# Performance work log

Hardware: AMD Instinct MI355X
Metric: run time of the kernel (lower is better)

Reference implementation:

```python
import jax, jax.numpy as jnp
import numpy as np

R = 2          # pool ratio -> context window = R * P
P = 8          # patch_size
STRIDE = 8     # window_stride
NH = 8         # n_heads
EPS = 1e-6


def _partition_nonoverlap(x, ws):
    # (N,C,H,W) -> (N*nH*nW, C, ws, ws), matches F.unfold path with padding 0
    n, c, h, w = x.shape
    x = x.reshape(n, c, h // ws, ws, w // ws, ws)
    x = jnp.transpose(x, (0, 2, 4, 1, 3, 5))
    return x.reshape(-1, c, ws, ws)


def _partition_overlap(x, ws, stride):
    # (N,C,H,W) -> (N*nH*nW, C, ws, ws) with padding (ws-stride)//2, matching F.unfold
    n, c, h, w = x.shape
    pad = (ws - stride) // 2
    xp = jnp.pad(x, ((0, 0), (0, 0), (pad, pad), (pad, pad)))
    ih = (jnp.arange(h // stride) * stride)[:, None] + jnp.arange(ws)[None, :]
    iw = (jnp.arange(w // stride) * stride)[:, None] + jnp.arange(ws)[None, :]
    xw = xp[:, :, ih, :]          # (n, c, nH, ws, Wp)
    xw = xw[:, :, :, :, iw]       # (n, c, nH, ws, nW, ws)
    xw = jnp.transpose(xw, (0, 2, 4, 1, 3, 5))  # (n, nH, nW, c, ws, ws)
    return xw.reshape(-1, c, ws, ws)


def setup_inputs() -> dict:
    key = jax.random.key(0)
    ks = jax.random.split(key, 4)
    C = 512
    x = jax.random.normal(ks[0], (1, C, 128, 128), jnp.float32)
    ln_w = jnp.ones((C,), jnp.float32)
    ln_b = jnp.zeros((C,), jnp.float32)
    mix_w = jax.random.normal(ks[1], (NH, P * P, P * P), jnp.float32) * 0.02
    mix_b = jnp.zeros((NH, P * P), jnp.float32)
    in_w = jax.random.normal(ks[2], (3 * C, C), jnp.float32) * 0.02
    in_b = jnp.zeros((3 * C,), jnp.float32)
    out_w = jax.random.normal(ks[3], (C, C), jnp.float32) * 0.02
    out_b = jnp.zeros((C,), jnp.float32)
    return dict(x=x, ln_w=ln_w, ln_b=ln_b, mix_w=mix_w, mix_b=mix_b,
                in_w=in_w, in_b=in_b, out_w=out_w, out_b=out_b)


def reference(x, ln_w, ln_b, mix_w, mix_b, in_w, in_b, out_w, out_b):
    n, c, h, w = x.shape
    ws = R * P
    L = P * P  # 64 positions per window

    # query windows: non-overlapping 8x8 patches -> (B, L, C)
    q = _partition_nonoverlap(x, P)
    q = q.reshape(-1, c, L).transpose(0, 2, 1)

    # context windows: 16x16 overlapping, avg-pooled r x r -> 8x8 -> (B, L, C)
    ctx = _partition_overlap(x, ws, STRIDE)
    ctx = ctx.reshape(-1, c, P, R, P, R).mean(axis=(3, 5))  # AvgPool2d(r, r)
    ctx = ctx.reshape(-1, c, L).transpose(0, 2, 1)

    # LayerNorm over channel dim (eps 1e-6, biased variance)
    mu = ctx.mean(-1, keepdims=True)
    var = ctx.var(-1, keepdims=True)
    ctx = (ctx - mu) / jnp.sqrt(var + EPS) * ln_w + ln_b

    # PositionMixing: per-head Linear(64,64) over the L axis + residual
    B = ctx.shape[0]
    t = ctx.transpose(0, 2, 1).reshape(B, NH, c // NH, L)  # (B, H, hd, L)
    mixed = jnp.einsum('bhcl,hml->bhcm', t, mix_w) + mix_b[None, :, None, :]
    ctx = (t + mixed).reshape(B, c, L).transpose(0, 2, 1)  # (B, L, C)

    # nn.MultiheadAttention with batch_first=False (torch default):
    # first dim B (windows) is the SEQUENCE, second dim L=64 is the BATCH.
    hd = c // NH
    Wq, Wk, Wv = in_w[:c], in_w[c:2 * c], in_w[2 * c:]
    bq, bk, bv = in_b[:c], in_b[c:2 * c], in_b[2 * c:]
    Q = (jnp.einsum('slc,ec->sle', q, Wq) + bq).reshape(B, L, NH, hd)
    K = (jnp.einsum('slc,ec->sle', ctx, Wk) + bk).reshape(B, L, NH, hd)
    V = (jnp.einsum('slc,ec->sle', ctx, Wv) + bv).reshape(B, L, NH, hd)
    scale = 1.0 / jnp.sqrt(jnp.asarray(hd, x.dtype))
    scores = jnp.einsum('slhd,tlhd->lhst', Q, K) * scale  # (L, H, B, B)
    attn = jax.nn.softmax(scores, axis=-1)
    o = jnp.einsum('lhst,tlhd->slhd', attn, V).reshape(B, L, c)
    o = jnp.einsum('slc,ec->sle', o, out_w) + out_b

    # nlc_to_nchw + window_reverse -> (N, C, H, W)
    o = o.transpose(0, 2, 1).reshape(B, c, P, P)
    o = o.reshape(n, h // P, w // P, c, P, P)
    o = jnp.transpose(o, (0, 3, 1, 4, 2, 5)).reshape(n, c, h, w)
    return o
```

## Files before the change

### kernel.cpp

```cpp
#include <hip/hip_runtime.h>


typedef __bf16 bf16;
typedef __bf16 bf16x2 __attribute__((ext_vector_type(2)));
typedef __bf16 bf16x4 __attribute__((ext_vector_type(4)));
typedef __bf16 bf16x8 __attribute__((ext_vector_type(8)));
typedef float f32x4 __attribute__((ext_vector_type(4)));

#define MFMA(a, b, c) __builtin_amdgcn_mfma_f32_16x16x32_bf16(a, b, c, 0, 0, 0)

__device__ __forceinline__ void gll16(const void* g, void* l) {
  __builtin_amdgcn_global_load_lds((const __attribute__((address_space(1))) void*)g,
                                   (__attribute__((address_space(3))) void*)l, 16, 0, 0);
}

__global__ void k_wconv(const float* __restrict__ in_w, const float* __restrict__ out_w,
                        bf16* __restrict__ wib, bf16* __restrict__ wob) {
  int i = blockIdx.x * blockDim.x + threadIdx.x;
  const int n1 = (1536 * 512) / 4;
  float4 v;
  bf16* dst;
  if (i < n1) { v = ((const float4*)in_w)[i];      dst = wib + (size_t)i * 4; }
  else        { v = ((const float4*)out_w)[i - n1]; dst = wob + (size_t)(i - n1) * 4; }
  dst[0] = (bf16)v.x; dst[1] = (bf16)v.y; dst[2] = (bf16)v.z; dst[3] = (bf16)v.w;
}

__global__ __launch_bounds__(256) void k_pq(const float* __restrict__ x,
                                            float* __restrict__ xp2t,
                                            bf16* __restrict__ qb) {
  __shared__ float xs[2][64][133];
  const int y2 = blockIdx.x, c0 = blockIdx.y * 64, t = threadIdx.x;
  #pragma unroll
  for (int it = 0; it < 16; ++it) {
    int flat = it * 256 + t;
    int ci = flat >> 6, rest = flat & 63;
    int yb = rest >> 5, xq = rest & 31;
    float4 v = *(const float4*)(x + (size_t)(c0 + ci) * 16384 +
                                (size_t)(2 * y2 + yb) * 128 + xq * 4);
    float* d = &xs[yb][ci][xq * 4];
    d[0] = v.x; d[1] = v.y; d[2] = v.z; d[3] = v.w;
  }
  __syncthreads();
  #pragma unroll
  for (int it = 0; it < 16; ++it) {
    int flat = it * 256 + t;
    int x2 = flat >> 6, ci = flat & 63;
    float s = xs[0][ci][2 * x2] + xs[0][ci][2 * x2 + 1] +
              xs[1][ci][2 * x2] + xs[1][ci][2 * x2 + 1];
    xp2t[(size_t)(y2 * 64 + x2) * 512 + c0 + ci] = 0.25f * s;
  }
  #pragma unroll
  for (int yb = 0; yb < 2; ++yb) {
    const int Y = 2 * y2 + yb;
    const int hy = Y >> 3, py = Y & 7;
    #pragma unroll
    for (int it = 0; it < 32; ++it) {
      int flat = it * 256 + t;
      int X = flat >> 6, ci = flat & 63;
      int l = py * 8 + (X & 7), s = hy * 16 + (X >> 3);
      qb[((size_t)l * 256 + s) * 512 + c0 + ci] = (bf16)xs[yb][ci][X];
    }
  }
}

__global__ __launch_bounds__(512) void k_ln(const float* __restrict__ xp2t,
                                            const float* __restrict__ lnw,
                                            const float* __restrict__ lnb,
                                            bf16* __restrict__ T) {
  __shared__ bf16 Tt[512][24];
  const int s = blockIdx.x, qt = blockIdx.y;
  const int wy = s >> 4, wx = s & 15;
  const int t = threadIdx.x, wv = t >> 6, ln = t & 63;

  float wl[8], bl[8];
  #pragma unroll
  for (int k = 0; k < 8; ++k) { wl[k] = lnw[k * 64 + ln]; bl[k] = lnb[k * 64 + ln]; }

  float v[2][8], mu_[2], rs_[2];
  #pragma unroll
  for (int p = 0; p < 2; ++p) {
    const int l = qt * 16 + wv * 2 + p;
    const int py = l >> 3, px = l & 7;
    const int y2 = wy * 4 - 2 + py, x2 = wx * 4 - 2 + px;
    const bool inb = (y2 >= 0) && (y2 < 64) && (x2 >= 0) && (x2 < 64);
    const float* src = xp2t + (size_t)(y2 * 64 + x2) * 512;
    float sum = 0.f, ssq = 0.f;
    #pragma unroll
    for (int k = 0; k < 8; ++k) {
      float xv = 0.f;
      if (inb) xv = src[k * 64 + ln];
      v[p][k] = xv; sum += xv; ssq += xv * xv;
    }
    #pragma unroll
    for (int off = 1; off < 64; off <<= 1) {
      sum += __shfl_xor(sum, off);
      ssq += __shfl_xor(ssq, off);
    }
    float mu = sum * (1.f / 512.f);
    mu_[p] = mu;
    rs_[p] = rsqrtf(ssq * (1.f / 512.f) - mu * mu + 1e-6f);
  }
  #pragma unroll
  for (int k = 0; k < 8; ++k) {
    const int c = k * 64 + ln;
    bf16x2 u;
    u.x = (bf16)((v[0][k] - mu_[0]) * rs_[0] * wl[k] + bl[k]);
    u.y = (bf16)((v[1][k] - mu_[1]) * rs_[1] * wl[k] + bl[k]);
    *(bf16x2*)(&Tt[c][wv * 2]) = u;
  }
  __syncthreads();
  #pragma unroll
  for (int it = 0; it < 2; ++it) {
    int flat = it * 512 + t;
    int c = flat >> 1, ch = flat & 1;
    bf16x8 u = *(const bf16x8*)(&Tt[c][ch * 8]);
    *(bf16x8*)(T + ((size_t)s * 512 + c) * 64 + qt * 16 + ch * 8) = u;
  }
}

__global__ __launch_bounds__(256) void k_mix(const bf16* __restrict__ T,
                                             const float* __restrict__ mix_w,
                                             const float* __restrict__ mix_b,
                                             bf16* __restrict__ ctx) {
  const int t = threadIdx.x, wv = t >> 6, ln = t & 63;
  const int s = blockIdx.x, hg = blockIdx.y;
  const int h = hg * 4 + wv;
  const int q = ln >> 4, r = ln & 15;

  bf16x8 a[4][2];
  #pragma unroll
  for (int m = 0; m < 4; ++m) {
    #pragma unroll
    for (int ks = 0; ks < 2; ++ks) {
      const int rm = m * 16 + r;
      const float* wsrc = mix_w + ((size_t)h * 64 + rm) * 64 + ks * 32 + q * 8;
      bf16x8 pk;
      #pragma unroll
      for (int e = 0; e < 8; ++e) {
        int l = ks * 32 + q * 8 + e;
        float w = wsrc[e] + (rm == l ? 1.f : 0.f);
        pk[e] = (bf16)w;
      }
      a[m][ks] = pk;
    }
  }
  const bf16* Tb = T + ((size_t)s * 512 + h * 64) * 64;
  bf16x8 b[4][2];
  #pragma unroll
  for (int n = 0; n < 4; ++n) {
    #pragma unroll
    for (int ks = 0; ks < 2; ++ks)
      b[n][ks] = *(const bf16x8*)(Tb + (size_t)(n * 16 + r) * 64 + ks * 32 + q * 8);
  }
  f32x4 acc[4][4] = {};
  #pragma unroll
  for (int ks = 0; ks < 2; ++ks) {
    #pragma unroll
    for (int m = 0; m < 4; ++m) {
      #pragma unroll
      for (int n = 0; n < 4; ++n) acc[m][n] = MFMA(a[m][ks], b[n][ks], acc[m][n]);
    }
  }
  #pragma unroll
  for (int m = 0; m < 4; ++m) {
    #pragma unroll
    for (int j = 0; j < 4; ++j) {
      const int rm = m * 16 + q * 4 + j;
      const float bias = mix_b[h * 64 + rm];
      #pragma unroll
      for (int n = 0; n < 4; ++n)
        ctx[((size_t)rm * 256 + s) * 512 + h * 64 + n * 16 + r] =
            (bf16)(acc[m][n][j] + bias);
    }
  }
}

__global__ __launch_bounds__(256, 4) void k_gemmQKV(const bf16* __restrict__ qb,
                                                    const bf16* __restrict__ ctxb,
                                                    const bf16* __restrict__ wib,
                                                    const float* __restrict__ in_b,
                                                    bf16* __restrict__ Qa,
                                                    bf16* __restrict__ Ka,
                                                    bf16* __restrict__ Vt) {
  __shared__ bf16 As[8192];
  __shared__ bf16 Bs[8192];
  const int t = threadIdx.x, wv = t >> 6, ln = t & 63;
  const int bm = blockIdx.x, bny = blockIdx.y;
  const bool isQ = (bny < 4);
  const int bn = isQ ? bny : bny - 4;
  const bf16* A = isQ ? qb : ctxb;
  const bf16* B = isQ ? wib : wib + 512 * 512;
  const float* bias = isQ ? in_b : in_b + 512;
  const int wm = wv >> 1, wn = wv & 1;
  const int q = ln >> 4, r = ln & 15;
  f32x4 acc[4][4] = {};

  const int srow = wv * 8 + (ln >> 3);
  const int swzc = (ln & 7) ^ (ln >> 3);
  const char* ga = (const char*)A + ((size_t)(bm * 128 + srow) * 512) * 2 + swzc * 16;
  const char* gb = (const char*)B + ((size_t)(bn * 128 + srow) * 512) * 2 + swzc * 16;

  for (int k0 = 0; k0 < 512; k0 += 64) {
    #pragma unroll
    for (int i = 0; i < 4; ++i) {
      gll16(ga + (size_t)i * 32 * 1024 + k0 * 2, As + i * 2048 + wv * 512);
      gll16(gb + (size_t)i * 32 * 1024 + k0 * 2, Bs + i * 2048 + wv * 512);
    }
    __syncthreads();
    #pragma unroll
    for (int ks = 0; ks < 2; ++ks) {
      bf16x8 af[4], bfr[4];
      #pragma unroll
      for (int m = 0; m < 4; ++m)
        af[m] = *(const bf16x8*)(As + (wm * 64 + m * 16 + r) * 64 +
                                 (((ks * 4 + q) ^ (r & 7)) * 8));
      #pragma unroll
      for (int n = 0; n < 4; ++n)
        bfr[n] = *(const bf16x8*)(Bs + (wn * 64 + n * 16 + r) * 64 +
                                  (((ks * 4 + q) ^ (r & 7)) * 8));
      #pragma unroll
      for (int m = 0; m < 4; ++m) {
        #pragma unroll
        for (int n = 0; n < 4; ++n) acc[m][n] = MFMA(af[m], bfr[n], acc[m][n]);
      }
    }
    __syncthreads();
  }

  const int r0 = bm * 128 + wm * 64 + q * 4;
  const int c0 = bn * 128 + wn * 64 + r;
  #pragma unroll
  for (int m = 0; m < 4; ++m) {
    const int rg0 = r0 + m * 16;
    const int li = rg0 >> 8;
    #pragma unroll
    for (int n = 0; n < 4; ++n) {
      const int cg = c0 + n * 16;
      const float bv = bias[cg];
      if (isQ) {
        #pragma unroll
        for (int j = 0; j < 4; ++j) {
          int sp = (rg0 + j) & 255;
          Qa[(((size_t)li * 8 + (cg >> 6)) * 256 + sp) * 64 + (cg & 63)] =
              (bf16)(acc[m][n][j] + bv);
        }
      } else if (cg < 512) {
        #pragma unroll
        for (int j = 0; j < 4; ++j) {
          int sp = (rg0 + j) & 255;
          Ka[(((size_t)li * 8 + (cg >> 6)) * 256 + sp) * 64 + (cg & 63)] =
              (bf16)(acc[m][n][j] + bv);
        }
      } else {
        const int e = cg - 512, hh = e >> 6, d = e & 63;
        const int sp = rg0 & 255;
        bf16x4 pk;
        #pragma unroll
        for (int j = 0; j < 4; ++j) pk[j] = (bf16)(acc[m][n][j] + bv);
        *(bf16x4*)(&Vt[(((size_t)li * 8 + hh) * 64 + d) * 256 + sp]) = pk;
      }
    }
  }
}

__global__ __launch_bounds__(256, 4) void k_gemmO(const bf16* __restrict__ A,
                                                  const bf16* __restrict__ B,
                                                  const float* __restrict__ bias,
                                                  bf16* __restrict__ O0) {
  __shared__ bf16 As[8192];
  __shared__ bf16 Bs[8192];
  const int t = threadIdx.x, wv = t >> 6, ln = t & 63;
  const int bm = blockIdx.x, bn = blockIdx.y;
  const int wm = wv >> 1, wn = wv & 1;
  const int q = ln >> 4, r = ln & 15;
  f32x4 acc[4][4] = {};

  const int srow = wv * 8 + (ln >> 3);
  const int swzc = (ln & 7) ^ (ln >> 3);
  const char* ga = (const char*)A + ((size_t)(bm * 128 + srow) * 512) * 2 + swzc * 16;
  const char* gb = (const char*)B + ((size_t)(bn * 128 + srow) * 512) * 2 + swzc * 16;

  for (int k0 = 0; k0 < 512; k0 += 64) {
    #pragma unroll
    for (int i = 0; i < 4; ++i) {
      gll16(ga + (size_t)i * 32 * 1024 + k0 * 2, As + i * 2048 + wv * 512);
      gll16(gb + (size_t)i * 32 * 1024 + k0 * 2, Bs + i * 2048 + wv * 512);
    }
    __syncthreads();
    #pragma unroll
    for (int ks = 0; ks < 2; ++ks) {
      bf16x8 af[4], bfr[4];
      #pragma unroll
      for (int m = 0; m < 4; ++m)
        af[m] = *(const bf16x8*)(As + (wm * 64 + m * 16 + r) * 64 +
                                 (((ks * 4 + q) ^ (r & 7)) * 8));
      #pragma unroll
      for (int n = 0; n < 4; ++n)
        bfr[n] = *(const bf16x8*)(Bs + (wn * 64 + n * 16 + r) * 64 +
                                  (((ks * 4 + q) ^ (r & 7)) * 8));
      #pragma unroll
      for (int m = 0; m < 4; ++m) {
        #pragma unroll
        for (int n = 0; n < 4; ++n) acc[m][n] = MFMA(af[m], bfr[n], acc[m][n]);
      }
    }
    __syncthreads();
  }

  const int r0 = bm * 128 + wm * 64 + q * 4;
  const int c0 = bn * 128 + wn * 64 + r;
  #pragma unroll
  for (int m = 0; m < 4; ++m) {
    const int rg0 = r0 + m * 16;
    #pragma unroll
    for (int n = 0; n < 4; ++n) {
      const int cg = c0 + n * 16;
      const float bv = bias[cg];
      #pragma unroll
      for (int j = 0; j < 4; ++j)
        O0[(size_t)(rg0 + j) * 512 + cg] = (bf16)(acc[m][n][j] + bv);
    }
  }
}

__global__ __launch_bounds__(256, 4) void k_attn(const bf16* __restrict__ Qa,
                                                 const bf16* __restrict__ Ka,
                                                 const bf16* __restrict__ Vt,
                                                 bf16* __restrict__ Oa) {
  __shared__ bf16 Ks[128][68];
  __shared__ bf16 Ps[64][132];
  __shared__ float sfl[64];
  __shared__ float rrs[64];

  const int t = threadIdx.x, wv = t >> 6, ln = t & 63;
  const int q = ln >> 4, r = ln & 15;
  const int bid = blockIdx.x;
  const int st = (bid >> 3) & 3;
  const int lh = (bid & 7) | ((bid >> 5) << 3);
  const int s0 = st * 64;
  const size_t base = (size_t)lh * (256 * 64);
  const bf16* Qlh = Qa + base;
  const bf16* Klh = Ka + base;
  const bf16* Vlh = Vt + base;

  const float SC = 0.125f * 1.4426950408889634f;

  bf16x8 aq[2];
  #pragma unroll
  for (int ks = 0; ks < 2; ++ks)
    aq[ks] = *(const bf16x8*)(Qlh + (size_t)(s0 + wv * 16 + r) * 64 + ks * 32 + q * 8);

  const int krow = t >> 1, khf = (t & 1) * 32;
  {
    bf16x8 kst0[4];
    #pragma unroll
    for (int i = 0; i < 4; ++i)
      kst0[i] = *(const bf16x8*)(Klh + (size_t)krow * 64 + khf + i * 8);
    #pragma unroll
    for (int i = 0; i < 4; ++i) *(bf16x8*)(&Ks[krow][khf + i * 8]) = kst0[i];
  }
  __syncthreads();

  f32x4 ao[4] = {};
  float m4[4], l4[4];
  f32x4 acc[8];

  #pragma unroll
  for (int n = 0; n < 8; ++n) acc[n] = (f32x4){0.f, 0.f, 0.f, 0.f};
  __builtin_amdgcn_s_setprio(1);
  #pragma unroll
  for (int n = 0; n < 8; ++n) {
    bf16x8 b0 = *(const bf16x8*)(&Ks[n * 16 + r][q * 8]);
    bf16x8 b1 = *(const bf16x8*)(&Ks[n * 16 + r][32 + q * 8]);
    acc[n] = MFMA(aq[0], b0, acc[n]);
    acc[n] = MFMA(aq[1], b1, acc[n]);
  }
  __builtin_amdgcn_s_setprio(0);

  bf16x8 bv[4];
  #pragma unroll
  for (int ks = 0; ks < 4; ++ks)
    bv[ks] = *(const bf16x8*)(Vlh + (size_t)(wv * 16 + r) * 256 + ks * 32 + q * 8);
  bf16x8 kst[4];
  #pragma unroll
  for (int i = 0; i < 4; ++i)
    kst[i] = *(const bf16x8*)(Klh + (size_t)(128 + krow) * 64 + khf + i * 8);

  #pragma unroll
  for (int j = 0; j < 4; ++j) {
    float mx = acc[0][j];
    #pragma unroll
    for (int n = 1; n < 8; ++n) mx = fmaxf(mx, acc[n][j]);
    #pragma unroll
    for (int off = 1; off < 16; off <<= 1) mx = fmaxf(mx, __shfl_xor(mx, off));
    m4[j] = mx;
    const float ms = mx * SC;
    float sm = 0.f;
    #pragma unroll
    for (int n = 0; n < 8; ++n) {
      float p = exp2f(acc[n][j] * SC - ms);
      acc[n][j] = p;
      sm += p;
    }
    #pragma unroll
    for (int off = 1; off < 16; off <<= 1) sm += __shfl_xor(sm, off);
    l4[j] = sm;
    const int row = wv * 16 + q * 4 + j;
    #pragma unroll
    for (int n = 0; n < 8; ++n) Ps[row][n * 16 + r] = (bf16)acc[n][j];
  }
  __syncthreads();

  #pragma unroll
  for (int i = 0; i < 4; ++i) *(bf16x8*)(&Ks[krow][khf + i * 8]) = kst[i];
  __builtin_amdgcn_s_setprio(1);
  #pragma unroll
  for (int ks = 0; ks < 4; ++ks) {
    #pragma unroll
    for (int m = 0; m < 4; ++m) {
      bf16x8 ap = *(const bf16x8*)(&Ps[m * 16 + r][ks * 32 + q * 8]);
      ao[m] = MFMA(ap, bv[ks], ao[m]);
    }
  }
  __builtin_amdgcn_s_setprio(0);
  __syncthreads();

  #pragma unroll
  for (int n = 0; n < 8; ++n) acc[n] = (f32x4){0.f, 0.f, 0.f, 0.f};
  __builtin_amdgcn_s_setprio(1);
  #pragma unroll
  for (int n = 0; n < 8; ++n) {
    bf16x8 b0 = *(const bf16x8*)(&Ks[n * 16 + r][q * 8]);
    bf16x8 b1 = *(const bf16x8*)(&Ks[n * 16 + r][32 + q * 8]);
    acc[n] = MFMA(aq[0], b0, acc[n]);
    acc[n] = MFMA(aq[1], b1, acc[n]);
  }
  __builtin_amdgcn_s_setprio(0);
  #pragma unroll
  for (int ks = 0; ks < 4; ++ks)
    bv[ks] = *(const bf16x8*)(Vlh + (size_t)(wv * 16 + r) * 256 + 128 + ks * 32 + q * 8);

  float sf4[4], rr4[4];
  #pragma unroll
  for (int j = 0; j < 4; ++j) {
    float mx = acc[0][j];
    #pragma unroll
    for (int n = 1; n < 8; ++n) mx = fmaxf(mx, acc[n][j]);
    #pragma unroll
    for (int off = 1; off < 16; off <<= 1) mx = fmaxf(mx, __shfl_xor(mx, off));
    const float mn = fmaxf(m4[j], mx);
    const float sf = exp2f((m4[j] - mn) * SC);
    const float ms = mn * SC;
    float sm = 0.f;
    #pragma unroll
    for (int n = 0; n < 8; ++n) {
      float p = exp2f(acc[n][j] * SC - ms);
      acc[n][j] = p;
      sm += p;
    }
    #pragma unroll
    for (int off = 1; off < 16; off <<= 1) sm += __shfl_xor(sm, off);
    sf4[j] = sf;
    rr4[j] = 1.f / (l4[j] * sf + sm);
    const int row = wv * 16 + q * 4 + j;
    #pragma unroll
    for (int n = 0; n < 8; ++n) Ps[row][n * 16 + r] = (bf16)acc[n][j];
  }
  if (r == 0) {
    *(f32x4*)(&sfl[wv * 16 + q * 4]) = (f32x4){sf4[0], sf4[1], sf4[2], sf4[3]};
    *(f32x4*)(&rrs[wv * 16 + q * 4]) = (f32x4){rr4[0], rr4[1], rr4[2], rr4[3]};
  }
  __syncthreads();

  #pragma unroll
  for (int m = 0; m < 4; ++m) {
    f32x4 sv = *(const f32x4*)(&sfl[m * 16 + q * 4]);
    #pragma unroll
    for (int j = 0; j < 4; ++j) ao[m][j] *= sv[j];
  }
  __builtin_amdgcn_s_setprio(1);
  #pragma unroll
  for (int ks = 0; ks < 4; ++ks) {
    #pragma unroll
    for (int m = 0; m < 4; ++m) {
      bf16x8 ap = *(const bf16x8*)(&Ps[m * 16 + r][ks * 32 + q * 8]);
      ao[m] = MFMA(ap, bv[ks], ao[m]);
    }
  }
  __builtin_amdgcn_s_setprio(0);

  float(*FS)[68] = (float(*)[68])(&Ks[0][0]);
  #pragma unroll
  for (int m = 0; m < 4; ++m) {
    f32x4 rv = *(const f32x4*)(&rrs[m * 16 + q * 4]);
    #pragma unroll
    for (int j = 0; j < 4; ++j)
      FS[m * 16 + q * 4 + j][wv * 16 + r] = ao[m][j] * rv[j];
  }
  __syncthreads();

  {
    const int row = t >> 2, qq = t & 3;
    const float* srcp = &FS[row][qq * 16];
    bf16x8 o0, o1;
    #pragma unroll
    for (int i = 0; i < 8; ++i) o0[i] = (bf16)srcp[i];
    #pragma unroll
    for (int i = 0; i < 8; ++i) o1[i] = (bf16)srcp[8 + i];
    bf16* dst = Oa + ((size_t)(lh >> 3) * 256 + s0 + row) * 512 + (lh & 7) * 64 + qq * 16;
    *(bf16x8*)(dst) = o0;
    *(bf16x8*)(dst + 8) = o1;
  }
}

__global__ void k_orelay(const bf16* __restrict__ o_tmp, float* __restrict__ out) {
  __shared__ bf16 buf[64][130];
  const int hy = blockIdx.x, py = blockIdx.y, e0 = blockIdx.z * 64, t = threadIdx.x;
  #pragma unroll
  for (int i = 0; i < 32; ++i) {
    int flat = i * 256 + t;
    int r = flat >> 6, e = flat & 63;
    int px = r >> 4, hx = r & 15;
    buf[e][hx * 8 + px] =
        o_tmp[((size_t)(py * 8 + px) * 256 + hy * 16 + hx) * 512 + e0 + e];
  }
  __syncthreads();
  const int Y = hy * 8 + py;
  #pragma unroll
  for (int i = 0; i < 32; ++i) {
    int flat = i * 256 + t;
    int e = flat >> 7, X = flat & 127;
    out[(size_t)(e0 + e) * 16384 + (size_t)Y * 128 + X] = (float)buf[e][X];
  }
}

extern "C" void kernel_launch(void* const* d_in, const int* in_sizes, int n_in,
                              void* d_out, int out_size, void* d_ws, size_t ws_size,
                              hipStream_t stream) {
  const float* x     = (const float*)d_in[0];
  const float* ln_w  = (const float*)d_in[1];
  const float* ln_b  = (const float*)d_in[2];
  const float* mix_w = (const float*)d_in[3];
  const float* mix_b = (const float*)d_in[4];
  const float* in_w  = (const float*)d_in[5];
  const float* in_b  = (const float*)d_in[6];
  const float* out_w = (const float*)d_in[7];
  const float* out_b = (const float*)d_in[8];
  float* out = (float*)d_out;
  char* ws = (char*)d_ws;

  const size_t MB = 1u << 20;
  float* xp2t = (float*)(ws);
  bf16* qb    = (bf16*)(ws + 8 * MB);
  bf16* Tn    = (bf16*)(ws + 24 * MB);
  bf16* ctxb  = (bf16*)(ws + 40 * MB);
  bf16* Qa    = (bf16*)(ws + 56 * MB);
  bf16* Ka    = (bf16*)(ws);
  bf16* Vt    = (bf16*)(ws + 16 * MB);
  bf16* oatt  = (bf16*)(ws + 32 * MB);
  bf16* otmp  = (bf16*)(ws + 48 * MB);
  bf16* wib   = (bf16*)(ws + 72 * MB);
  bf16* wob   = (bf16*)(ws + 72 * MB + 1572864);

  k_wconv<<<1024, 256, 0, stream>>>(in_w, out_w, wib, wob);
  k_pq<<<dim3(64, 8), 256, 0, stream>>>(x, xp2t, qb);
  k_ln<<<dim3(256, 4), 512, 0, stream>>>(xp2t, ln_w, ln_b, Tn);
  k_mix<<<dim3(256, 2), 256, 0, stream>>>(Tn, mix_w, mix_b, ctxb);
  k_gemmQKV<<<dim3(128, 12), 256, 0, stream>>>(qb, ctxb, wib, in_b, Qa, Ka, Vt);
  k_attn<<<2048, 256, 0, stream>>>(Qa, Ka, Vt, oatt);
  k_gemmO<<<dim3(128, 4), 256, 0, stream>>>(oatt, wob, out_b, otmp);
  k_orelay<<<dim3(16, 8, 8), 256, 0, stream>>>(otmp, out);
}
```

Measured before the change: 133.2 us.

## Double-buffer LDS tiles in QKV and output projection GEMMs

Both projection GEMM kernels now use two LDS buffers, issuing the global-to-LDS loads for the next K tile before computing on the current one. This overlaps memory latency with MFMA work and leaves one barrier per iteration instead of two. Shared memory per block doubles to 64KB, and launch bounds drop from 4 to 2 blocks per CU, which cuts occupancy.

```diff
diff --git a/kernel.cpp b/kernel.cpp
--- a/kernel.cpp
+++ b/kernel.cpp
@@ -175,15 +175,15 @@
   }
 }
 
-__global__ __launch_bounds__(256, 4) void k_gemmQKV(const bf16* __restrict__ qb,
+__global__ __launch_bounds__(256, 2) void k_gemmQKV(const bf16* __restrict__ qb,
                                                     const bf16* __restrict__ ctxb,
                                                     const bf16* __restrict__ wib,
                                                     const float* __restrict__ in_b,
                                                     bf16* __restrict__ Qa,
                                                     bf16* __restrict__ Ka,
                                                     bf16* __restrict__ Vt) {
-  __shared__ bf16 As[8192];
-  __shared__ bf16 Bs[8192];
+  __shared__ bf16 As[2][8192];
+  __shared__ bf16 Bs[2][8192];
   const int t = threadIdx.x, wv = t >> 6, ln = t & 63;
   const int bm = blockIdx.x, bny = blockIdx.y;
   const bool isQ = (bny < 4);
@@ -200,23 +200,33 @@
   const char* ga = (const char*)A + ((size_t)(bm * 128 + srow) * 512) * 2 + swzc * 16;
   const char* gb = (const char*)B + ((size_t)(bn * 128 + srow) * 512) * 2 + swzc * 16;
 
-  for (int k0 = 0; k0 < 512; k0 += 64) {
-    #pragma unroll
-    for (int i = 0; i < 4; ++i) {
-      gll16(ga + (size_t)i * 32 * 1024 + k0 * 2, As + i * 2048 + wv * 512);
-      gll16(gb + (size_t)i * 32 * 1024 + k0 * 2, Bs + i * 2048 + wv * 512);
-    }
-    __syncthreads();
+  #pragma unroll
+  for (int i = 0; i < 4; ++i) {
+    gll16(ga + (size_t)i * 32 * 1024, As[0] + i * 2048 + wv * 512);
+    gll16(gb + (size_t)i * 32 * 1024, Bs[0] + i * 2048 + wv * 512);
+  }
+  __syncthreads();
+
+  int cur = 0;
+  for (int kt = 0; kt < 8; ++kt) {
+    if (kt < 7) {
+      const int k0 = (kt + 1) * 64;
+      #pragma unroll
+      for (int i = 0; i < 4; ++i) {
+        gll16(ga + (size_t)i * 32 * 1024 + k0 * 2, As[cur ^ 1] + i * 2048 + wv * 512);
+        gll16(gb + (size_t)i * 32 * 1024 + k0 * 2, Bs[cur ^ 1] + i * 2048 + wv * 512);
+      }
+    }
     #pragma unroll
     for (int ks = 0; ks < 2; ++ks) {
       bf16x8 af[4], bfr[4];
       #pragma unroll
       for (int m = 0; m < 4; ++m)
-        af[m] = *(const bf16x8*)(As + (wm * 64 + m * 16 + r) * 64 +
+        af[m] = *(const bf16x8*)(As[cur] + (wm * 64 + m * 16 + r) * 64 +
                                  (((ks * 4 + q) ^ (r & 7)) * 8));
       #pragma unroll
       for (int n = 0; n < 4; ++n)
-        bfr[n] = *(const bf16x8*)(Bs + (wn * 64 + n * 16 + r) * 64 +
+        bfr[n] = *(const bf16x8*)(Bs[cur] + (wn * 64 + n * 16 + r) * 64 +
                                   (((ks * 4 + q) ^ (r & 7)) * 8));
       #pragma unroll
       for (int m = 0; m < 4; ++m) {
@@ -225,6 +235,7 @@
       }
     }
     __syncthreads();
+    cur ^= 1;
   }
 
   const int r0 = bm * 128 + wm * 64 + q * 4;
@@ -263,12 +274,12 @@
   }
 }
 
-__global__ __launch_bounds__(256, 4) void k_gemmO(const bf16* __restrict__ A,
+__global__ __launch_bounds__(256, 2) void k_gemmO(const bf16* __restrict__ A,
                                                   const bf16* __restrict__ B,
                                                   const float* __restrict__ bias,
                                                   bf16* __restrict__ O0) {
-  __shared__ bf16 As[8192];
-  __shared__ bf16 Bs[8192];
+  __shared__ bf16 As[2][8192];
+  __shared__ bf16 Bs[2][8192];
   const int t = threadIdx.x, wv = t >> 6, ln = t & 63;
   const int bm = blockIdx.x, bn = blockIdx.y;
   const int wm = wv >> 1, wn = wv & 1;
@@ -280,23 +291,33 @@
   const char* ga = (const char*)A + ((size_t)(bm * 128 + srow) * 512) * 2 + swzc * 16;
   const char* gb = (const char*)B + ((size_t)(bn * 128 + srow) * 512) * 2 + swzc * 16;
 
-  for (int k0 = 0; k0 < 512; k0 += 64) {
-    #pragma unroll
-    for (int i = 0; i < 4; ++i) {
-      gll16(ga + (size_t)i * 32 * 1024 + k0 * 2, As + i * 2048 + wv * 512);
-      gll16(gb + (size_t)i * 32 * 1024 + k0 * 2, Bs + i * 2048 + wv * 512);
-    }
-    __syncthreads();
+  #pragma unroll
+  for (int i = 0; i < 4; ++i) {
+    gll16(ga + (size_t)i * 32 * 1024, As[0] + i * 2048 + wv * 512);
+    gll16(gb + (size_t)i * 32 * 1024, Bs[0] + i * 2048 + wv * 512);
+  }
+  __syncthreads();
+
+  int cur = 0;
+  for (int kt = 0; kt < 8; ++kt) {
+    if (kt < 7) {
+      const int k0 = (kt + 1) * 64;
+      #pragma unroll
+      for (int i = 0; i < 4; ++i) {
+        gll16(ga + (size_t)i * 32 * 1024 + k0 * 2, As[cur ^ 1] + i * 2048 + wv * 512);
+        gll16(gb + (size_t)i * 32 * 1024 + k0 * 2, Bs[cur ^ 1] + i * 2048 + wv * 512);
+      }
+    }
     #pragma unroll
     for (int ks = 0; ks < 2; ++ks) {
       bf16x8 af[4], bfr[4];
       #pragma unroll
       for (int m = 0; m < 4; ++m)
-        af[m] = *(const bf16x8*)(As + (wm * 64 + m * 16 + r) * 64 +
+        af[m] = *(const bf16x8*)(As[cur] + (wm * 64 + m * 16 + r) * 64 +
                                  (((ks * 4 + q) ^ (r & 7)) * 8));
       #pragma unroll
       for (int n = 0; n < 4; ++n)
-        bfr[n] = *(const bf16x8*)(Bs + (wn * 64 + n * 16 + r) * 64 +
+        bfr[n] = *(const bf16x8*)(Bs[cur] + (wn * 64 + n * 16 + r) * 64 +
                                   (((ks * 4 + q) ^ (r & 7)) * 8));
       #pragma unroll
       for (int m = 0; m < 4; ++m) {
@@ -305,6 +326,7 @@
       }
     }
     __syncthreads();
+    cur ^= 1;
   }
 
   const int r0 = bm * 128 + wm * 64 + q * 4;
```

Measured after the change: 140.8 us. +5.7%, slower.

## Pipeline GEMM K-loop with triple-buffered LDS and async prefetch

Applied to the files above, without the earlier changes.

Replaces the load-sync-compute-sync K loop in the QKV and output-projection GEMMs with a shared core that uses three LDS stages of 32-wide K tiles. Each stage is prefetched two iterations ahead using global_load_lds, with vmcnt waits and a single barrier per iteration. Warps are split so two load A and two load B, and a new 2-bit swizzle is used. This aims to hide global load latency behind MFMA work, at the cost of more LDS per block, which is why the launch-bounds occupancy hint drops from 4 to 3.

```diff
diff --git a/kernel.cpp b/kernel.cpp
--- a/kernel.cpp
+++ b/kernel.cpp
@@ -175,15 +175,82 @@
   }
 }
 
-__global__ __launch_bounds__(256, 4) void k_gemmQKV(const bf16* __restrict__ qb,
+template <typename EPI>
+__device__ __forceinline__ void gemm_pipe_core(const bf16* __restrict__ A,
+                                               const bf16* __restrict__ B,
+                                               int bm, int bn, bf16* As, bf16* Bs,
+                                               f32x4 (&acc)[4][4]) {
+  const int t = threadIdx.x, wv = t >> 6, ln = t & 63;
+  const int wm = wv >> 1, wn = wv & 1;
+  const int q = ln >> 4, r = ln & 15;
+
+  const bf16* G = (wv < 2) ? A : B;
+  const int gbase = ((wv < 2) ? bm : bn) * 128;
+  const int srow0 = (wv & 1) * 64 + (ln >> 2);
+  const int slotp = (ln & 3) ^ ((ln >> 2) & 3) ^ ((ln >> 4) & 3);
+  const char* gsrc = (const char*)G + ((size_t)(gbase + srow0) * 512) * 2 + slotp * 16;
+  bf16* lbase = (wv < 2) ? As : Bs;
+  const int lchunk0 = (wv & 1) * 4;
+
+  const int swzr = (r & 3) ^ ((r >> 2) & 3);
+
+#define STAGE(kt, b)                                                          \
+  {                                                                           \
+    const char* gk = gsrc + (size_t)(kt) * 64;                                \
+    _Pragma("unroll")                                                         \
+    for (int i = 0; i < 4; ++i)                                               \
+      gll16(gk + (size_t)i * 16 * 1024, lbase + (b) * 4096 + (lchunk0 + i) * 512); \
+  }
+
+#define COMPUTE(b)                                                            \
+  {                                                                           \
+    bf16x8 af[4], bfr[4];                                                     \
+    _Pragma("unroll")                                                         \
+    for (int m = 0; m < 4; ++m)                                               \
+      af[m] = *(const bf16x8*)(As + (b) * 4096 +                              \
+                               (wm * 64 + m * 16 + r) * 32 + (q ^ swzr) * 8); \
+    _Pragma("unroll")                                                         \
+    for (int n = 0; n < 4; ++n)                                               \
+      bfr[n] = *(const bf16x8*)(Bs + (b) * 4096 +                             \
+                                (wn * 64 + n * 16 + r) * 32 + (q ^ swzr) * 8);\
+    _Pragma("unroll")                                                         \
+    for (int m = 0; m < 4; ++m) {                                             \
+      _Pragma("unroll")                                                       \
+      for (int n = 0; n < 4; ++n) acc[m][n] = MFMA(af[m], bfr[n], acc[m][n]); \
+    }                                                                         \
+  }
+
+  STAGE(0, 0);
+  STAGE(1, 1);
+  int b = 0;
+  for (int kt = 0; kt < 15; ++kt) {
+    asm volatile("s_waitcnt vmcnt(4)" ::: "memory");
+    __builtin_amdgcn_s_barrier();
+    if (kt < 14) {
+      const int b2 = (kt + 2) % 3;
+      STAGE(kt + 2, b2);
+    }
+    COMPUTE(b);
+    b = (b + 1) % 3;
+  }
+  asm volatile("s_waitcnt vmcnt(0)" ::: "memory");
+  __builtin_amdgcn_s_barrier();
+  COMPUTE(b);
+#undef STAGE
+#undef COMPUTE
+}
+
+struct EpiNull {};
+
+__global__ __launch_bounds__(256, 3) void k_gemmQKV(const bf16* __restrict__ qb,
                                                     const bf16* __restrict__ ctxb,
                                                     const bf16* __restrict__ wib,
                                                     const float* __restrict__ in_b,
                                                     bf16* __restrict__ Qa,
                                                     bf16* __restrict__ Ka,
                                                     bf16* __restrict__ Vt) {
-  __shared__ bf16 As[8192];
-  __shared__ bf16 Bs[8192];
+  __shared__ bf16 As[3 * 4096];
+  __shared__ bf16 Bs[3 * 4096];
   const int t = threadIdx.x, wv = t >> 6, ln = t & 63;
   const int bm = blockIdx.x, bny = blockIdx.y;
   const bool isQ = (bny < 4);
@@ -195,37 +262,7 @@
   const int q = ln >> 4, r = ln & 15;
   f32x4 acc[4][4] = {};
 
-  const int srow = wv * 8 + (ln >> 3);
-  const int swzc = (ln & 7) ^ (ln >> 3);
-  const char* ga = (const char*)A + ((size_t)(bm * 128 + srow) * 512) * 2 + swzc * 16;
-  const char* gb = (const char*)B + ((size_t)(bn * 128 + srow) * 512) * 2 + swzc * 16;
-
-  for (int k0 = 0; k0 < 512; k0 += 64) {
-    #pragma unroll
-    for (int i = 0; i < 4; ++i) {
-      gll16(ga + (size_t)i * 32 * 1024 + k0 * 2, As + i * 2048 + wv * 512);
-      gll16(gb + (size_t)i * 32 * 1024 + k0 * 2, Bs + i * 2048 + wv * 512);
-    }
-    __syncthreads();
-    #pragma unroll
-    for (int ks = 0; ks < 2; ++ks) {
-      bf16x8 af[4], bfr[4];
-      #pragma unroll
-      for (int m = 0; m < 4; ++m)
-        af[m] = *(const bf16x8*)(As + (wm * 64 + m * 16 + r) * 64 +
-                                 (((ks * 4 + q) ^ (r & 7)) * 8));
-      #pragma unroll
-      for (int n = 0; n < 4; ++n)
-        bfr[n] = *(const bf16x8*)(Bs + (wn * 64 + n * 16 + r) * 64 +
-                                  (((ks * 4 + q) ^ (r & 7)) * 8));
-      #pragma unroll
-      for (int m = 0; m < 4; ++m) {
-        #pragma unroll
-        for (int n = 0; n < 4; ++n) acc[m][n] = MFMA(af[m], bfr[n], acc[m][n]);
-      }
-    }
-    __syncthreads();
-  }
+  gemm_pipe_core<EpiNull>(A, B, bm, bn, As, Bs, acc);
 
   const int r0 = bm * 128 + wm * 64 + q * 4;
   const int c0 = bn * 128 + wn * 64 + r;
@@ -263,49 +300,19 @@
   }
 }
 
-__global__ __launch_bounds__(256, 4) void k_gemmO(const bf16* __restrict__ A,
+__global__ __launch_bounds__(256, 3) void k_gemmO(const bf16* __restrict__ A,
                                                   const bf16* __restrict__ B,
                                                   const float* __restrict__ bias,
                                                   bf16* __restrict__ O0) {
-  __shared__ bf16 As[8192];
-  __shared__ bf16 Bs[8192];
+  __shared__ bf16 As[3 * 4096];
+  __shared__ bf16 Bs[3 * 4096];
   const int t = threadIdx.x, wv = t >> 6, ln = t & 63;
   const int bm = blockIdx.x, bn = blockIdx.y;
   const int wm = wv >> 1, wn = wv & 1;
   const int q = ln >> 4, r = ln & 15;
   f32x4 acc[4][4] = {};
 
-  const int srow = wv * 8 + (ln >> 3);
-  const int swzc = (ln & 7) ^ (ln >> 3);
-  const char* ga = (const char*)A + ((size_t)(bm * 128 + srow) * 512) * 2 + swzc * 16;
-  const char* gb = (const char*)B + ((size_t)(bn * 128 + srow) * 512) * 2 + swzc * 16;
-
-  for (int k0 = 0; k0 < 512; k0 += 64) {
-    #pragma unroll
-    for (int i = 0; i < 4; ++i) {
-      gll16(ga + (size_t)i * 32 * 1024 + k0 * 2, As + i * 2048 + wv * 512);
-      gll16(gb + (size_t)i * 32 * 1024 + k0 * 2, Bs + i * 2048 + wv * 512);
-    }
-    __syncthreads();
-    #pragma unroll
-    for (int ks = 0; ks < 2; ++ks) {
-      bf16x8 af[4], bfr[4];
-      #pragma unroll
-      for (int m = 0; m < 4; ++m)
-        af[m] = *(const bf16x8*)(As + (wm * 64 + m * 16 + r) * 64 +
-                                 (((ks * 4 + q) ^ (r & 7)) * 8));
-      #pragma unroll
-      for (int n = 0; n < 4; ++n)
-        bfr[n] = *(const bf16x8*)(Bs + (wn * 64 + n * 16 + r) * 64 +
-                                  (((ks * 4 + q) ^ (r & 7)) * 8));
-      #pragma unroll
-      for (int m = 0; m < 4; ++m) {
-        #pragma unroll
-        for (int n = 0; n < 4; ++n) acc[m][n] = MFMA(af[m], bfr[n], acc[m][n]);
-      }
-    }
-    __syncthreads();
-  }
+  gemm_pipe_core<EpiNull>(A, B, bm, bn, As, Bs, acc);
 
   const int r0 = bm * 128 + wm * 64 + q * 4;
   const int c0 = bn * 128 + wn * 64 + r;
```

Result: slower. 138.6 us (+4.1%).
